# Performance work log

Measured on AMD Instinct MI355X. Metric: run time of the kernel, lower is better.

The kernel has to match this reference:

```python
import jax, jax.numpy as jnp
import numpy as np

D_Z, D_A = 128, 64
D = D_Z + D_A            # 192
H1, H2 = 512, 512
E, S = 16, 1
B, N = 64, 2048
LN_EPS = 1e-5


def mish(x):
    return x * jnp.tanh(jax.nn.softplus(x))


def layernorm(x, g, b):
    m = jnp.mean(x, axis=-1, keepdims=True)
    v = jnp.mean((x - m) ** 2, axis=-1, keepdims=True)
    return (x - m) * jax.lax.rsqrt(v + LN_EPS) * g + b


def setup_inputs() -> dict:
    key = jax.random.key(0)
    ks = jax.random.split(key, 12)
    inp = {
        "z": jax.random.normal(ks[0], (B, N, D_Z), jnp.float32),
        "a": jax.random.normal(ks[1], (B, N, D_A), jnp.float32),
        "phi": jax.random.normal(ks[2], (D, E, S), jnp.float32) / np.sqrt(D),
        # stacked per-expert params (vectorized over e)
        "W1": jax.random.normal(ks[3], (E, D, H1), jnp.float32) / np.sqrt(D),
        "b1": jnp.zeros((E, H1), jnp.float32),
        "g1": jnp.ones((E, H1), jnp.float32),
        "be1": jnp.zeros((E, H1), jnp.float32),
        "W2": jax.random.normal(ks[4], (E, H1, H2), jnp.float32) / np.sqrt(H1),
        "b2": jnp.zeros((E, H2), jnp.float32),
        "g2": jnp.ones((E, H2), jnp.float32),
        "be2": jnp.zeros((E, H2), jnp.float32),
        "W3": jax.random.normal(ks[5], (E, H2, D_Z), jnp.float32) / np.sqrt(H2),
        "b3": jnp.zeros((E, D_Z), jnp.float32),
    }
    return inp


def reference(z, a, phi, W1, b1, g1, be1, W2, b2, g2, be2, W3, b3):
    x = jnp.concatenate([z, a], axis=-1)                      # [B,N,D]
    weights = jnp.einsum('bnd,des->bnes', x, phi)             # [B,N,E,S]
    dispatch = jax.nn.softmax(weights, axis=1)                # over tokens N
    xin = jnp.einsum('bnes,bnd->besd', dispatch, x)           # [B,E,S,D]
    # batched per-expert MLP: NormedLinear -> NormedLinear -> Linear
    h = jnp.einsum('besd,edh->besh', xin, W1) + b1[None, :, None, :]
    h = mish(layernorm(h, g1[None, :, None, :], be1[None, :, None, :]))
    h = jnp.einsum('besh,ehk->besk', h, W2) + b2[None, :, None, :]
    h = mish(layernorm(h, g2[None, :, None, :], be2[None, :, None, :]))
    out_e = jnp.einsum('besk,ekz->besz', h, W3) + b3[None, :, None, :]
    expert_outputs = out_e.reshape(out_e.shape[0], E * S, D_Z)    # b (e s) z
    combine = jax.nn.softmax(weights.reshape(weights.shape[0], weights.shape[1], E * S), axis=-1)
    out = jnp.einsum('bnk,bkz->bnz', combine, expert_outputs)     # [B,N,d_z]
    return out
```

## Files before the change

kernel.cpp:

```cpp
#include <hip/hip_runtime.h>
#include <math.h>

#define BB 64
#define NN 2048
#define DZ 128
#define DA 64
#define DD 192
#define EE 16
#define HH 512
#define LN_EPS 1e-5f
#define NCH 64

typedef __attribute__((ext_vector_type(8))) short short8;
typedef __attribute__((ext_vector_type(4))) float f32x4;

__device__ __forceinline__ float mishf(float x) {
    float sp = (x > 20.f) ? x : log1pf(__expf(x));
    return x * tanhf(sp);
}

__device__ __forceinline__ unsigned short bf16_rne(float f) {
    unsigned u = __float_as_uint(f);
    return (unsigned short)((u + 0x7FFFu + ((u >> 16) & 1u)) >> 16);
}
__device__ __forceinline__ float bf16f(unsigned short h) {
    return __uint_as_float(((unsigned)h) << 16);
}

__global__ __launch_bounds__(256)
void k_phipack(const float* __restrict__ phi, unsigned short* __restrict__ ph,
               unsigned short* __restrict__ pl) {
    int idx = blockIdx.x * 256 + threadIdx.x;
    if (idx >= 6 * 64 * 8) return;
    int j = idx & 7, lane = (idx >> 3) & 63, kk = idx >> 9;
    int e = lane & 15, g = lane >> 4;
    int d = kk * 32 + g * 8 + j;
    float f = phi[d * EE + e];
    unsigned short h = bf16_rne(f);
    ph[idx] = h;
    pl[idx] = bf16_rne(f - bf16f(h));
}

__global__ __launch_bounds__(256)
void k_wxin(const float* __restrict__ z, const float* __restrict__ a,
            const unsigned short* __restrict__ php,
            const unsigned short* __restrict__ plp,
            float* __restrict__ w, float* __restrict__ pxin,
            float* __restrict__ pZ) {
    __shared__ unsigned int xhl[4 * 32 * 49];
    __shared__ float wexp[32 * 17];
    int ch = blockIdx.x, b = blockIdx.y;
    int t = threadIdx.x, wv = t >> 6, l = t & 63;
    int g = l >> 4, c = l & 15;
    long tok0 = (long)b * NN + (long)ch * 32;

    {
        const float4* zp = (const float4*)(z + tok0 * DZ);
        const float4* ap = (const float4*)(a + tok0 * DA);
#pragma unroll
        for (int k = 0; k < 6; k++) {
            int f = t + k * 256;
            int tok = f / 48, q = f - tok * 48;
            float4 v = (q < 32) ? zp[tok * 32 + q] : ap[tok * 16 + (q - 32)];
            int reg = q / 12;
            int dq = q * 4 - reg * 48;
            unsigned* dst = &xhl[(reg * 32 + tok) * 49 + dq];
            const float* pv = &v.x;
#pragma unroll
            for (int i = 0; i < 4; i++) {
                unsigned short h = bf16_rne(pv[i]);
                unsigned short lo = bf16_rne(pv[i] - bf16f(h));
                dst[i] = ((unsigned)h << 16) | (unsigned)lo;
            }
        }
    }
    __syncthreads();

    short8 xh0, xl0, xh1, xl1, xh2, xl2;
#pragma unroll
    for (int j = 0; j < 8; j++) {
        int rowb = (wv * 32 + g * 8 + j) * 49;
        unsigned u0 = xhl[rowb + c];
        unsigned u1 = xhl[rowb + 16 + c];
        unsigned u2 = xhl[rowb + 32 + c];
        xh0[j] = (short)(u0 >> 16); xl0[j] = (short)(u0 & 0xffff);
        xh1[j] = (short)(u1 >> 16); xl1[j] = (short)(u1 & 0xffff);
        xh2[j] = (short)(u2 >> 16); xl2[j] = (short)(u2 & 0xffff);
    }

    if (wv < 2) {
        f32x4 accw = {0.f, 0.f, 0.f, 0.f};
#pragma unroll
        for (int kk = 0; kk < 6; kk++) {
            short8 bh = *(const short8*)(php + kk * 512 + l * 8);
            short8 bl = *(const short8*)(plp + kk * 512 + l * 8);
            int dbase = kk * 32 + g * 8;
            int reg = dbase / 48;
            int dq = dbase - reg * 48;
            int rowb = (reg * 32 + wv * 16 + c) * 49 + dq;
            short8 ah, al;
#pragma unroll
            for (int j = 0; j < 8; j++) {
                unsigned u = xhl[rowb + j];
                ah[j] = (short)(u >> 16);
                al[j] = (short)(u & 0xffff);
            }
            accw = __builtin_amdgcn_mfma_f32_16x16x32_bf16(ah, bh, accw, 0, 0, 0);
            accw = __builtin_amdgcn_mfma_f32_16x16x32_bf16(al, bh, accw, 0, 0, 0);
            accw = __builtin_amdgcn_mfma_f32_16x16x32_bf16(ah, bl, accw, 0, 0, 0);
        }
#pragma unroll
        for (int r = 0; r < 4; r++) {
            long row_g = tok0 + wv * 16 + g * 4 + r;
            w[row_g * EE + c] = accw[r];
            wexp[(wv * 16 + g * 4 + r) * 17 + c] = __expf(accw[r]);
        }
    }
    __syncthreads();

    short8 ad;
    float zl = 0.f;
#pragma unroll
    for (int j = 0; j < 8; j++) {
        float wf = wexp[(g * 8 + j) * 17 + c];
        ad[j] = (short)bf16_rne(wf);
        zl += wf;
    }
    f32x4 acc0 = {0.f, 0.f, 0.f, 0.f};
    f32x4 acc1 = {0.f, 0.f, 0.f, 0.f};
    f32x4 acc2 = {0.f, 0.f, 0.f, 0.f};
    acc0 = __builtin_amdgcn_mfma_f32_16x16x32_bf16(ad, xh0, acc0, 0, 0, 0);
    acc0 = __builtin_amdgcn_mfma_f32_16x16x32_bf16(ad, xl0, acc0, 0, 0, 0);
    acc1 = __builtin_amdgcn_mfma_f32_16x16x32_bf16(ad, xh1, acc1, 0, 0, 0);
    acc1 = __builtin_amdgcn_mfma_f32_16x16x32_bf16(ad, xl1, acc1, 0, 0, 0);
    acc2 = __builtin_amdgcn_mfma_f32_16x16x32_bf16(ad, xh2, acc2, 0, 0, 0);
    acc2 = __builtin_amdgcn_mfma_f32_16x16x32_bf16(ad, xl2, acc2, 0, 0, 0);

    if (wv == 0) {
        zl += __shfl_xor(zl, 16);
        zl += __shfl_xor(zl, 32);
        if (l < 16) pZ[((long)ch * BB + b) * EE + c] = zl;
    }

    float* pb = pxin + (long)ch * (EE * BB * DD) + (long)b * DD;
#pragma unroll
    for (int r = 0; r < 4; r++) {
        int e = g * 4 + r;
        float* pr = pb + (long)e * (BB * DD);
        pr[(wv * 3 + 0) * 16 + c] = acc0[r];
        pr[(wv * 3 + 1) * 16 + c] = acc1[r];
        pr[(wv * 3 + 2) * 16 + c] = acc2[r];
    }
}

__global__ __launch_bounds__(256)
void k_zred(const float* __restrict__ pZ, float* __restrict__ Zg) {
    int idx = blockIdx.x * 256 + threadIdx.x;
    if (idx >= BB * EE) return;
    float s = 0.f;
#pragma unroll 8
    for (int ch = 0; ch < NCH; ch++)
        s += pZ[(long)ch * (BB * EE) + idx];
    Zg[idx] = 1.f / s;
}

__global__ __launch_bounds__(256)
void k_xinred(const float* __restrict__ pxin, const float* __restrict__ Zg,
              float* __restrict__ xin) {
    long i = (long)blockIdx.x * 256 + threadIdx.x;
    int e = (int)(i / (BB * DD));
    int rem = (int)(i - (long)e * (BB * DD));
    int b = rem / DD;
    float s = 0.f;
#pragma unroll 8
    for (int ch = 0; ch < NCH; ch++)
        s += pxin[(long)ch * (EE * BB * DD) + i];
    xin[i] = s * Zg[b * EE + e];
}

__global__ __launch_bounds__(256)
void k_weights(const float* __restrict__ z, const float* __restrict__ a,
               const unsigned short* __restrict__ php,
               const unsigned short* __restrict__ plp,
               float* __restrict__ w) {
    int t = threadIdx.x;
    int wv = t >> 6, l = t & 63;
    long tokbase = ((long)blockIdx.x * 4 + wv) * 16;
    long tokA = tokbase + (l & 15);
    int g = l >> 4;

    short8 bh[6], bl[6], ah[6], al[6];
#pragma unroll
    for (int kk = 0; kk < 6; kk++) {
        bh[kk] = *(const short8*)(php + kk * 512 + l * 8);
        bl[kk] = *(const short8*)(plp + kk * 512 + l * 8);
    }
#pragma unroll
    for (int kk = 0; kk < 6; kk++) {
        int d0 = kk * 32 + g * 8;
        const float* src = (d0 < DZ) ? (z + tokA * DZ + d0)
                                     : (a + tokA * DA + (d0 - DZ));
        float4 v0 = ((const float4*)src)[0];
        float4 v1 = ((const float4*)src)[1];
        float f[8] = {v0.x, v0.y, v0.z, v0.w, v1.x, v1.y, v1.z, v1.w};
#pragma unroll
        for (int j = 0; j < 8; j++) {
            unsigned short h = bf16_rne(f[j]);
            ah[kk][j] = (short)h;
            al[kk][j] = (short)bf16_rne(f[j] - bf16f(h));
        }
    }
    f32x4 acc = {0.f, 0.f, 0.f, 0.f};
#pragma unroll
    for (int kk = 0; kk < 6; kk++)
        acc = __builtin_amdgcn_mfma_f32_16x16x32_bf16(ah[kk], bh[kk], acc, 0, 0, 0);
#pragma unroll
    for (int kk = 0; kk < 6; kk++)
        acc = __builtin_amdgcn_mfma_f32_16x16x32_bf16(al[kk], bh[kk], acc, 0, 0, 0);
#pragma unroll
    for (int kk = 0; kk < 6; kk++)
        acc = __builtin_amdgcn_mfma_f32_16x16x32_bf16(ah[kk], bl[kk], acc, 0, 0, 0);
    int e = l & 15;
#pragma unroll
    for (int r = 0; r < 4; r++) {
        long row = tokbase + g * 4 + r;
        w[row * EE + e] = acc[r];
    }
}

#define RSTR 17
__global__ __launch_bounds__(256)
void k_stats1(const float* __restrict__ w, float* __restrict__ lmax,
              float* __restrict__ lsum) {
    __shared__ float red[256 * RSTR];
    int b = blockIdx.y, c = blockIdx.x, t = threadIdx.x;
    const float* wb = w + ((long)b * NN + c * 512) * EE;
    float m[EE];
#pragma unroll
    for (int e = 0; e < EE; e++) m[e] = -1e30f;
    for (int k = 0; k < 2; k++) {
        const float4* row = (const float4*)(wb + ((long)(k * 256 + t)) * EE);
#pragma unroll
        for (int q = 0; q < 4; q++) {
            float4 v = row[q];
            m[q * 4 + 0] = fmaxf(m[q * 4 + 0], v.x);
            m[q * 4 + 1] = fmaxf(m[q * 4 + 1], v.y);
            m[q * 4 + 2] = fmaxf(m[q * 4 + 2], v.z);
            m[q * 4 + 3] = fmaxf(m[q * 4 + 3], v.w);
        }
    }
#pragma unroll
    for (int e = 0; e < EE; e++) red[t * RSTR + e] = m[e];
    __syncthreads();
    for (int s = 128; s > 0; s >>= 1) {
        if (t < s) {
#pragma unroll
            for (int e = 0; e < EE; e++)
                red[t * RSTR + e] = fmaxf(red[t * RSTR + e], red[(t + s) * RSTR + e]);
        }
        __syncthreads();
    }
    float mg[EE];
#pragma unroll
    for (int e = 0; e < EE; e++) mg[e] = red[e];
    __syncthreads();
    float s_[EE];
#pragma unroll
    for (int e = 0; e < EE; e++) s_[e] = 0.f;
    for (int k = 0; k < 2; k++) {
        const float4* row = (const float4*)(wb + ((long)(k * 256 + t)) * EE);
#pragma unroll
        for (int q = 0; q < 4; q++) {
            float4 v = row[q];
            s_[q * 4 + 0] += __expf(v.x - mg[q * 4 + 0]);
            s_[q * 4 + 1] += __expf(v.y - mg[q * 4 + 1]);
            s_[q * 4 + 2] += __expf(v.z - mg[q * 4 + 2]);
            s_[q * 4 + 3] += __expf(v.w - mg[q * 4 + 3]);
        }
    }
#pragma unroll
    for (int e = 0; e < EE; e++) red[t * RSTR + e] = s_[e];
    __syncthreads();
    for (int s = 128; s > 0; s >>= 1) {
        if (t < s) {
#pragma unroll
            for (int e = 0; e < EE; e++)
                red[t * RSTR + e] += red[(t + s) * RSTR + e];
        }
        __syncthreads();
    }
    if (t < EE) {
        lmax[((long)b * 4 + c) * EE + t] = mg[t];
        lsum[((long)b * 4 + c) * EE + t] = red[t];
    }
}

__global__ __launch_bounds__(256)
void k_stats2(const float* __restrict__ lmax, const float* __restrict__ lsum,
              float* __restrict__ gmax, float* __restrict__ grcp) {
    int idx = blockIdx.x * 256 + threadIdx.x;
    if (idx >= BB * EE) return;
    int b = idx >> 4, e = idx & 15;
    float gm = -1e30f;
#pragma unroll
    for (int c = 0; c < 4; c++)
        gm = fmaxf(gm, lmax[((long)b * 4 + c) * EE + e]);
    float Z = 0.f;
#pragma unroll
    for (int c = 0; c < 4; c++)
        Z += __expf(lmax[((long)b * 4 + c) * EE + e] - gm) * lsum[((long)b * 4 + c) * EE + e];
    gmax[idx] = gm;
    grcp[idx] = 1.f / Z;
}

__global__ __launch_bounds__(192)
void k_xin_scalar(const float* __restrict__ z, const float* __restrict__ a,
                  const float* __restrict__ w, const float* __restrict__ gmax,
                  const float* __restrict__ grcp, float* __restrict__ dst) {
    __shared__ float disp[128 * EE];
    int b = blockIdx.y, chunk = blockIdx.x, t = threadIdx.x;
    const float* wrow = w + ((long)b * NN + (long)chunk * 128) * EE;
    for (int i = t; i < 128 * EE; i += 192) {
        int e = i & 15;
        disp[i] = __expf(wrow[i] - gmax[b * EE + e]) * grcp[b * EE + e];
    }
    __syncthreads();
    const float* xp;
    int stride;
    if (t < DZ) { xp = z + ((long)b * NN + (long)chunk * 128) * DZ + t; stride = DZ; }
    else        { xp = a + ((long)b * NN + (long)chunk * 128) * DA + (t - DZ); stride = DA; }
    float acc[EE];
#pragma unroll
    for (int e = 0; e < EE; e++) acc[e] = 0.f;
    for (int n = 0; n < 128; n++) {
        float xv = xp[(long)n * stride];
        const float4* dp = (const float4*)(disp + n * EE);
#pragma unroll
        for (int q = 0; q < 4; q++) {
            float4 p = dp[q];
            acc[q * 4 + 0] += p.x * xv;
            acc[q * 4 + 1] += p.y * xv;
            acc[q * 4 + 2] += p.z * xv;
            acc[q * 4 + 3] += p.w * xv;
        }
    }
#pragma unroll
    for (int e = 0; e < EE; e++)
        atomicAdd(&dst[((long)e * BB + b) * DD + t], acc[e]);
}

template<int K, int OUT, int KSLICE, bool ADD_BIAS>
__global__ __launch_bounds__(256)
void k_gemm(const float* __restrict__ X, const float* __restrict__ W,
            const float* __restrict__ bias, float* __restrict__ Yp) {
    constexpr int SP = KSLICE + 4;
    constexpr int K4 = KSLICE / 4;
    __shared__ float xs[64 * SP];
    int cb = blockIdx.x, ks = blockIdx.y, e = blockIdx.z;
    int t = threadIdx.x;
    int k0 = ks * KSLICE;
    for (int i = t; i < 64 * K4; i += 256) {
        int r = i / K4, k4 = i % K4;
        *(float4*)&xs[r * SP + k4 * 4] =
            *(const float4*)(X + ((long)e * BB + r) * K + k0 + k4 * 4);
    }
    __syncthreads();
    int c = cb * 32 + (t & 7) * 4;
    int r0 = (t >> 3) * 2;
    const float* Wp = W + ((long)e * K + k0) * OUT + c;
    float acc0[4], acc1[4];
#pragma unroll
    for (int j = 0; j < 4; j++) {
        float bv = ADD_BIAS ? bias[(long)e * OUT + c + j] : 0.f;
        acc0[j] = bv;
        acc1[j] = bv;
    }
#pragma unroll 4
    for (int k4 = 0; k4 < K4; k4++) {
        float4 x0 = *(const float4*)&xs[r0 * SP + k4 * 4];
        float4 x1 = *(const float4*)&xs[(r0 + 1) * SP + k4 * 4];
        const float* xp0 = &x0.x;
        const float* xp1 = &x1.x;
#pragma unroll
        for (int j = 0; j < 4; j++) {
            float4 wv = *(const float4*)(Wp + (long)(k4 * 4 + j) * OUT);
            float xa = xp0[j], xb = xp1[j];
            acc0[0] += xa * wv.x; acc0[1] += xa * wv.y;
            acc0[2] += xa * wv.z; acc0[3] += xa * wv.w;
            acc1[0] += xb * wv.x; acc1[1] += xb * wv.y;
            acc1[2] += xb * wv.z; acc1[3] += xb * wv.w;
        }
    }
    float* yp = Yp + ((long)ks * (EE * BB) + (long)e * BB + r0) * OUT + c;
    *(float4*)yp         = make_float4(acc0[0], acc0[1], acc0[2], acc0[3]);
    *(float4*)(yp + OUT) = make_float4(acc1[0], acc1[1], acc1[2], acc1[3]);
}

template<int KS, bool HAS_BIAS>
__global__ __launch_bounds__(256)
void k_lnact(const float* __restrict__ Yp, const float* __restrict__ bias,
             const float* __restrict__ g, const float* __restrict__ be,
             float* __restrict__ Yo) {
    __shared__ float redS[4], redQ[4];
    int row = blockIdx.x, t = threadIdx.x;
    int e = row >> 6;
    float v[2];
#pragma unroll
    for (int j = 0; j < 2; j++) {
        int cj = t + j * 256;
        float s = HAS_BIAS ? bias[(long)e * HH + cj] : 0.f;
#pragma unroll
        for (int ks = 0; ks < KS; ks++)
            s += Yp[((long)ks * (EE * BB) + row) * HH + cj];
        v[j] = s;
    }
    float s = v[0] + v[1];
    float q = v[0] * v[0] + v[1] * v[1];
    for (int off = 32; off > 0; off >>= 1) {
        s += __shfl_xor(s, off);
        q += __shfl_xor(q, off);
    }
    int wave = t >> 6, lane = t & 63;
    if (lane == 0) { redS[wave] = s; redQ[wave] = q; }
    __syncthreads();
    float S = redS[0] + redS[1] + redS[2] + redS[3];
    float Q = redQ[0] + redQ[1] + redQ[2] + redQ[3];
    float mean = S * (1.f / HH);
    float var = Q * (1.f / HH) - mean * mean;
    float rstd = rsqrtf(var + LN_EPS);
#pragma unroll
    for (int j = 0; j < 2; j++) {
        int cj = t + j * 256;
        float gg = g[(long)e * HH + cj], bb = be[(long)e * HH + cj];
        Yo[(long)row * HH + cj] = mishf((v[j] - mean) * rstd * gg + bb);
    }
}

template<int KS>
__global__ __launch_bounds__(256)
void k_fin3(const float* __restrict__ p3, const float* __restrict__ b3,
            float* __restrict__ eout) {
    int t = threadIdx.x;
    int row = blockIdx.x * 2 + (t >> 7);
    int c = t & 127;
    int e = row >> 6, b = row & 63;
    float s = b3[(long)e * DZ + c];
#pragma unroll
    for (int ks = 0; ks < KS; ks++)
        s += p3[((long)ks * (EE * BB) + row) * DZ + c];
    eout[((long)b * EE + e) * DZ + c] = s;
}

__global__ __launch_bounds__(256)
void k_combine(const float* __restrict__ w, const float* __restrict__ eout,
               float* __restrict__ out) {
    __shared__ float comb[64][EE];
    __shared__ float eo[EE * DZ];
    int b = blockIdx.y, n0 = blockIdx.x * 64, t = threadIdx.x;
    for (int i = t; i < EE * DZ; i += 256) eo[i] = eout[(long)b * EE * DZ + i];
    int tok = t >> 2, sub = t & 3;
    const float4 wv = *(const float4*)(w + ((long)b * NN + n0 + tok) * EE + sub * 4);
    float mx = fmaxf(fmaxf(wv.x, wv.y), fmaxf(wv.z, wv.w));
    mx = fmaxf(mx, __shfl_xor(mx, 1, 4));
    mx = fmaxf(mx, __shfl_xor(mx, 2, 4));
    float e0 = __expf(wv.x - mx), e1 = __expf(wv.y - mx);
    float e2 = __expf(wv.z - mx), e3 = __expf(wv.w - mx);
    float s = e0 + e1 + e2 + e3;
    s += __shfl_xor(s, 1, 4);
    s += __shfl_xor(s, 2, 4);
    float rs = 1.f / s;
    comb[tok][sub * 4 + 0] = e0 * rs;
    comb[tok][sub * 4 + 1] = e1 * rs;
    comb[tok][sub * 4 + 2] = e2 * rs;
    comb[tok][sub * 4 + 3] = e3 * rs;
    __syncthreads();
    for (int i = t; i < 64 * DZ; i += 256) {
        int tk = i >> 7, c = i & 127;
        float acc = 0.f;
#pragma unroll
        for (int e = 0; e < EE; e++) acc += comb[tk][e] * eo[e * DZ + c];
        out[((long)b * NN + n0 + tk) * DZ + c] = acc;
    }
}

extern "C" void kernel_launch(void* const* d_in, const int* in_sizes, int n_in,
                              void* d_out, int out_size, void* d_ws, size_t ws_size,
                              hipStream_t stream) {
    const float* z   = (const float*)d_in[0];
    const float* a   = (const float*)d_in[1];
    const float* phi = (const float*)d_in[2];
    const float* W1  = (const float*)d_in[3];
    const float* b1  = (const float*)d_in[4];
    const float* g1  = (const float*)d_in[5];
    const float* be1 = (const float*)d_in[6];
    const float* W2  = (const float*)d_in[7];
    const float* b2  = (const float*)d_in[8];
    const float* g2  = (const float*)d_in[9];
    const float* be2 = (const float*)d_in[10];
    const float* W3  = (const float*)d_in[11];
    const float* b3  = (const float*)d_in[12];
    float* out = (float*)d_out;

    char* p = (char*)d_ws;
    float* w    = (float*)p; p += (size_t)BB * NN * EE * 4;
    float* gmax = (float*)p; p += (size_t)BB * EE * 4;
    float* grcp = (float*)p; p += (size_t)BB * EE * 4;
    float* lmax = (float*)p; p += (size_t)BB * 4 * EE * 4;
    float* lsum = (float*)p; p += (size_t)BB * 4 * EE * 4;
    float* xin  = (float*)p; p += (size_t)BB * EE * DD * 4;
    unsigned short* php = (unsigned short*)p; p += 6 * 64 * 8 * 2;
    unsigned short* plp = (unsigned short*)p; p += 6 * 64 * 8 * 2;
    float* pZ   = (float*)p; p += (size_t)NCH * BB * EE * 4;
    float* Zg   = (float*)p; p += (size_t)BB * EE * 4;
    char* region = p;
    float* pxin = (float*)region;
    float* part = (float*)region;
    float* h1   = (float*)(region + (size_t)4 * EE * BB * HH * 4);
    float* h2   = h1;
    float* eout = (float*)(region + (size_t)4 * EE * BB * HH * 4
                                  + (size_t)EE * BB * HH * 4);
    size_t region_off = (size_t)(region - (char*)d_ws);
    size_t need_full = region_off + (size_t)NCH * EE * BB * DD * 4;
    bool full = ws_size >= need_full;

    k_phipack<<<12, 256, 0, stream>>>(phi, php, plp);

    if (full) {
        k_wxin<<<dim3(NCH, BB), 256, 0, stream>>>(z, a, php, plp, w, pxin, pZ);
        k_zred<<<4, 256, 0, stream>>>(pZ, Zg);
        k_xinred<<<EE * BB * DD / 256, 256, 0, stream>>>(pxin, Zg, xin);
    } else {
        k_weights<<<BB * NN / 64, 256, 0, stream>>>(z, a, php, plp, w);
        k_stats1<<<dim3(4, BB), 256, 0, stream>>>(w, lmax, lsum);
        k_stats2<<<4, 256, 0, stream>>>(lmax, lsum, gmax, grcp);
        hipMemsetAsync(xin, 0, (size_t)BB * EE * DD * 4, stream);
        k_xin_scalar<<<dim3(NN / 128, BB), 192, 0, stream>>>(z, a, w, gmax, grcp, xin);
    }

    k_gemm<DD, HH, 96, false>
        <<<dim3(HH / 32, 2, EE), 256, 0, stream>>>(xin, W1, nullptr, part);
    k_lnact<2, true><<<EE * BB, 256, 0, stream>>>(part, b1, g1, be1, h1);

    k_gemm<HH, HH, 128, false>
        <<<dim3(HH / 32, 4, EE), 256, 0, stream>>>(h1, W2, nullptr, part);
    k_lnact<4, true><<<EE * BB, 256, 0, stream>>>(part, b2, g2, be2, h2);

    k_gemm<HH, DZ, 64, false>
        <<<dim3(DZ / 32, 8, EE), 256, 0, stream>>>(h2, W3, nullptr, part);
    k_fin3<8><<<EE * BB / 2, 256, 0, stream>>>(part, b3, eout);

    k_combine<<<dim3(NN / 64, BB), 256, 0, stream>>>(w, eout, out);
}
```

Measured before the change: 127.6 us.

## Process two token sub-chunks per block and halve partial xin chunks

Each block of the weights/xin kernel now covers 64 tokens as two 32-token sub-chunks, accumulating the dispatch-weighted xin in registers across both. The second sub-chunk's global load and bf16 split are issued after the first sub-chunk's operands are in registers, so the load overlaps the first MFMA stage. NCH drops from 64 to 32, halving the partial xin and Z buffers written to global memory and the work of reducing them downstream. The cost is fewer blocks in the grid, one extra barrier per block and more register pressure.

```diff
diff --git a/kernel.cpp b/kernel.cpp
--- a/kernel.cpp
+++ b/kernel.cpp
@@ -9,7 +9,7 @@
 #define EE 16
 #define HH 512
 #define LN_EPS 1e-5f
-#define NCH 64
+#define NCH 32
 
 typedef __attribute__((ext_vector_type(8))) short short8;
 typedef __attribute__((ext_vector_type(4))) float f32x4;
@@ -48,13 +48,13 @@
             float* __restrict__ w, float* __restrict__ pxin,
             float* __restrict__ pZ) {
     __shared__ unsigned int xhl[4 * 32 * 49];
-    __shared__ float wexp[32 * 17];
-    int ch = blockIdx.x, b = blockIdx.y;
+    __shared__ float wexp[2][32 * 17];
+    int ch2 = blockIdx.x, b = blockIdx.y;
     int t = threadIdx.x, wv = t >> 6, l = t & 63;
     int g = l >> 4, c = l & 15;
-    long tok0 = (long)b * NN + (long)ch * 32;
-
-    {
+
+    auto phase0 = [&](int s) {
+        long tok0 = (long)b * NN + (long)ch2 * 64 + s * 32;
         const float4* zp = (const float4*)(z + tok0 * DZ);
         const float4* ap = (const float4*)(a + tok0 * DA);
 #pragma unroll
@@ -73,76 +73,89 @@
                 dst[i] = ((unsigned)h << 16) | (unsigned)lo;
             }
         }
-    }
-    __syncthreads();
-
-    short8 xh0, xl0, xh1, xl1, xh2, xl2;
-#pragma unroll
-    for (int j = 0; j < 8; j++) {
-        int rowb = (wv * 32 + g * 8 + j) * 49;
-        unsigned u0 = xhl[rowb + c];
-        unsigned u1 = xhl[rowb + 16 + c];
-        unsigned u2 = xhl[rowb + 32 + c];
-        xh0[j] = (short)(u0 >> 16); xl0[j] = (short)(u0 & 0xffff);
-        xh1[j] = (short)(u1 >> 16); xl1[j] = (short)(u1 & 0xffff);
-        xh2[j] = (short)(u2 >> 16); xl2[j] = (short)(u2 & 0xffff);
-    }
-
-    if (wv < 2) {
-        f32x4 accw = {0.f, 0.f, 0.f, 0.f};
-#pragma unroll
-        for (int kk = 0; kk < 6; kk++) {
-            short8 bh = *(const short8*)(php + kk * 512 + l * 8);
-            short8 bl = *(const short8*)(plp + kk * 512 + l * 8);
-            int dbase = kk * 32 + g * 8;
-            int reg = dbase / 48;
-            int dq = dbase - reg * 48;
-            int rowb = (reg * 32 + wv * 16 + c) * 49 + dq;
-            short8 ah, al;
-#pragma unroll
-            for (int j = 0; j < 8; j++) {
-                unsigned u = xhl[rowb + j];
-                ah[j] = (short)(u >> 16);
-                al[j] = (short)(u & 0xffff);
-            }
-            accw = __builtin_amdgcn_mfma_f32_16x16x32_bf16(ah, bh, accw, 0, 0, 0);
-            accw = __builtin_amdgcn_mfma_f32_16x16x32_bf16(al, bh, accw, 0, 0, 0);
-            accw = __builtin_amdgcn_mfma_f32_16x16x32_bf16(ah, bl, accw, 0, 0, 0);
-        }
-#pragma unroll
-        for (int r = 0; r < 4; r++) {
-            long row_g = tok0 + wv * 16 + g * 4 + r;
-            w[row_g * EE + c] = accw[r];
-            wexp[(wv * 16 + g * 4 + r) * 17 + c] = __expf(accw[r]);
-        }
-    }
-    __syncthreads();
-
-    short8 ad;
-    float zl = 0.f;
-#pragma unroll
-    for (int j = 0; j < 8; j++) {
-        float wf = wexp[(g * 8 + j) * 17 + c];
-        ad[j] = (short)bf16_rne(wf);
-        zl += wf;
-    }
+    };
+
     f32x4 acc0 = {0.f, 0.f, 0.f, 0.f};
     f32x4 acc1 = {0.f, 0.f, 0.f, 0.f};
     f32x4 acc2 = {0.f, 0.f, 0.f, 0.f};
-    acc0 = __builtin_amdgcn_mfma_f32_16x16x32_bf16(ad, xh0, acc0, 0, 0, 0);
-    acc0 = __builtin_amdgcn_mfma_f32_16x16x32_bf16(ad, xl0, acc0, 0, 0, 0);
-    acc1 = __builtin_amdgcn_mfma_f32_16x16x32_bf16(ad, xh1, acc1, 0, 0, 0);
-    acc1 = __builtin_amdgcn_mfma_f32_16x16x32_bf16(ad, xl1, acc1, 0, 0, 0);
-    acc2 = __builtin_amdgcn_mfma_f32_16x16x32_bf16(ad, xh2, acc2, 0, 0, 0);
-    acc2 = __builtin_amdgcn_mfma_f32_16x16x32_bf16(ad, xl2, acc2, 0, 0, 0);
+    float zacc = 0.f;
+
+    phase0(0);
+    __syncthreads();
+
+#pragma unroll
+    for (int s = 0; s < 2; s++) {
+        long tok0 = (long)b * NN + (long)ch2 * 64 + s * 32;
+
+        short8 xh0, xl0, xh1, xl1, xh2, xl2;
+#pragma unroll
+        for (int j = 0; j < 8; j++) {
+            int rowb = (wv * 32 + g * 8 + j) * 49;
+            unsigned u0 = xhl[rowb + c];
+            unsigned u1 = xhl[rowb + 16 + c];
+            unsigned u2 = xhl[rowb + 32 + c];
+            xh0[j] = (short)(u0 >> 16); xl0[j] = (short)(u0 & 0xffff);
+            xh1[j] = (short)(u1 >> 16); xl1[j] = (short)(u1 & 0xffff);
+            xh2[j] = (short)(u2 >> 16); xl2[j] = (short)(u2 & 0xffff);
+        }
+
+        if (wv < 2) {
+            f32x4 accw = {0.f, 0.f, 0.f, 0.f};
+#pragma unroll
+            for (int kk = 0; kk < 6; kk++) {
+                short8 bh = *(const short8*)(php + kk * 512 + l * 8);
+                short8 bl = *(const short8*)(plp + kk * 512 + l * 8);
+                int dbase = kk * 32 + g * 8;
+                int reg = dbase / 48;
+                int dq = dbase - reg * 48;
+                int rowb = (reg * 32 + wv * 16 + c) * 49 + dq;
+                short8 ah, al;
+#pragma unroll
+                for (int j = 0; j < 8; j++) {
+                    unsigned u = xhl[rowb + j];
+                    ah[j] = (short)(u >> 16);
+                    al[j] = (short)(u & 0xffff);
+                }
+                accw = __builtin_amdgcn_mfma_f32_16x16x32_bf16(ah, bh, accw, 0, 0, 0);
+                accw = __builtin_amdgcn_mfma_f32_16x16x32_bf16(al, bh, accw, 0, 0, 0);
+                accw = __builtin_amdgcn_mfma_f32_16x16x32_bf16(ah, bl, accw, 0, 0, 0);
+            }
+#pragma unroll
+            for (int r = 0; r < 4; r++) {
+                long row_g = tok0 + wv * 16 + g * 4 + r;
+                w[row_g * EE + c] = accw[r];
+                wexp[s][(wv * 16 + g * 4 + r) * 17 + c] = __expf(accw[r]);
+            }
+        }
+        __syncthreads();
+
+        short8 ad;
+#pragma unroll
+        for (int j = 0; j < 8; j++) {
+            float wf = wexp[s][(g * 8 + j) * 17 + c];
+            ad[j] = (short)bf16_rne(wf);
+            if (wv == 0) zacc += wf;
+        }
+
+        if (s == 0) phase0(1);
+
+        acc0 = __builtin_amdgcn_mfma_f32_16x16x32_bf16(ad, xh0, acc0, 0, 0, 0);
+        acc0 = __builtin_amdgcn_mfma_f32_16x16x32_bf16(ad, xl0, acc0, 0, 0, 0);
+        acc1 = __builtin_amdgcn_mfma_f32_16x16x32_bf16(ad, xh1, acc1, 0, 0, 0);
+        acc1 = __builtin_amdgcn_mfma_f32_16x16x32_bf16(ad, xl1, acc1, 0, 0, 0);
+        acc2 = __builtin_amdgcn_mfma_f32_16x16x32_bf16(ad, xh2, acc2, 0, 0, 0);
+        acc2 = __builtin_amdgcn_mfma_f32_16x16x32_bf16(ad, xl2, acc2, 0, 0, 0);
+
+        if (s == 0) __syncthreads();
+    }
 
     if (wv == 0) {
-        zl += __shfl_xor(zl, 16);
-        zl += __shfl_xor(zl, 32);
-        if (l < 16) pZ[((long)ch * BB + b) * EE + c] = zl;
-    }
-
-    float* pb = pxin + (long)ch * (EE * BB * DD) + (long)b * DD;
+        zacc += __shfl_xor(zacc, 16);
+        zacc += __shfl_xor(zacc, 32);
+        if (l < 16) pZ[((long)ch2 * BB + b) * EE + c] = zacc;
+    }
+
+    float* pb = pxin + (long)ch2 * (EE * BB * DD) + (long)b * DD;
 #pragma unroll
     for (int r = 0; r < 4; r++) {
         int e = g * 4 + r;
```

After: 113.7 us. 10.9% less time.
